# Performance work log

Hardware: AMD Instinct MI355X
Metric: run time of the kernel (lower is better)

The kernel has to match this reference:

```python
import jax, jax.numpy as jnp
import numpy as np

EPS_NORM = 1e-12   # torch F.normalize eps
EPS_TRIP = 1e-6    # torch pairwise_distance eps
MARGIN = 1.0

def _l2_normalize(x, axis=1):
    n = jnp.linalg.norm(x, axis=axis, keepdims=True)
    return x / jnp.maximum(n, EPS_NORM)

def setup_inputs() -> dict:
    key = jax.random.key(0)
    k1, k2 = jax.random.split(key)
    bs, m, d = 32768, 2048, 256
    query = jax.random.normal(k1, (bs, d), dtype=jnp.float32)
    memory = jax.random.normal(k2, (m, d), dtype=jnp.float32)
    return {"query": query, "memory": memory}

def reference(query, memory):
    m, d = memory.shape
    q = _l2_normalize(query, axis=1)                      # [bs, d]
    score = jnp.matmul(q, memory.T)                       # [bs, m]
    sfx_score_query = jax.nn.softmax(score, axis=0)       # softmax over batch
    sfx_score_memory = jax.nn.softmax(score, axis=1)      # softmax over slots

    # --- update (note: original passes sfx_score_query for BOTH score args) ---
    max_idx = jnp.argmax(sfx_score_query, axis=1)         # [bs] topk(k=1) over dim=1
    colmax = jnp.max(sfx_score_query, axis=0)             # [m]
    sel = jnp.take_along_axis(sfx_score_query, max_idx[:, None], axis=1)[:, 0]  # score[j, max_idx[j]]
    w = sel / colmax[max_idx]                              # [bs]
    # vectorized form of the per-slot gather/weighted-sum loop (segment-sum)
    query_update = jax.ops.segment_sum(w[:, None] * q, max_idx, num_segments=m)  # [m, d]
    updated_memory = jax.lax.stop_gradient(_l2_normalize(query_update + memory, axis=1))

    # --- read (uses ORIGINAL memory in the train path) ---
    concat_memory = jnp.matmul(jax.lax.stop_gradient(sfx_score_memory), memory)  # [bs, d]
    update_query = jnp.concatenate([q, concat_memory], axis=1)                   # [bs, 2d]

    # --- losses (computed from sfx_score_memory as intended) ---
    top2_vals, top2_idx = jax.lax.top_k(sfx_score_memory, 2)
    pos = jax.lax.stop_gradient(memory[top2_idx[:, 0]])   # [bs, d]
    neg = jax.lax.stop_gradient(memory[top2_idx[:, 1]])   # [bs, d]
    gathering_loss = jnp.mean((q - pos) ** 2)
    d_pos = jnp.linalg.norm(q - pos + EPS_TRIP, axis=1)
    d_neg = jnp.linalg.norm(q - neg + EPS_TRIP, axis=1)
    spreading_loss = jnp.mean(jnp.maximum(d_pos - d_neg + MARGIN, 0.0))

    return (update_query, updated_memory, sfx_score_query, sfx_score_memory,
            gathering_loss, spreading_loss)
```

## Files before the change

kernel.cpp:

```cpp
#include <hip/hip_runtime.h>
#include <hip/hip_bf16.h>
#include <cstddef>
#include <cstdint>

#define BS 32768
#define MSLOT 2048
#define D 256
#define NCHUNK 128

typedef _Float16 f16;
typedef _Float16 f16x8 __attribute__((ext_vector_type(8)));
typedef float f32x4 __attribute__((ext_vector_type(4)));

#define WAITV(n) asm volatile("s_waitcnt vmcnt(" #n ")" ::: "memory")

__device__ __forceinline__ void barrier_raw() {
    asm volatile("" ::: "memory");
    __builtin_amdgcn_s_barrier();
    asm volatile("" ::: "memory");
}

__device__ __forceinline__ void lds_cp16(void* dst, const void* src) {
    __builtin_amdgcn_global_load_lds(
        (const __attribute__((address_space(1))) void*)src,
        (__attribute__((address_space(3))) void*)dst, 16, 0, 0);
}

__device__ __forceinline__ void top2_merge(float& a0, int& ai0, float& a1, int& ai1,
                                           float b0, int bi0, float b1, int bi1)
{
    bool bt = (b0 > a0) || (b0 == a0 && bi0 < ai0);
    float n0, n1; int ni0, ni1;
    if (bt) {
        n0 = b0; ni0 = bi0;
        bool s2 = (b1 > a0) || (b1 == a0 && bi1 < ai0);
        n1 = s2 ? b1 : a0; ni1 = s2 ? bi1 : ai0;
    } else {
        n0 = a0; ni0 = ai0;
        bool s2 = (b0 > a1) || (b0 == a1 && bi0 < ai1);
        n1 = s2 ? b0 : a1; ni1 = s2 ? bi0 : ai1;
    }
    a0 = n0; ai0 = ni0; a1 = n1; ai1 = ni1;
}

__global__ __launch_bounds__(256) void k_prepq(const float* __restrict__ query,
                                               float* __restrict__ out0,
                                               f16* __restrict__ qcat)
{
    __shared__ float sbuf[4];
    const int i = blockIdx.x, t = threadIdx.x;
    float v = query[(size_t)i * D + t];
    float ss = v * v;
#pragma unroll
    for (int off = 32; off; off >>= 1) ss += __shfl_xor(ss, off, 64);
    if ((t & 63) == 0) sbuf[t >> 6] = ss;
    __syncthreads();
    float tot = (sbuf[0] + sbuf[1]) + (sbuf[2] + sbuf[3]);
    float n = fmaxf(sqrtf(tot), 1e-12f);
    float qv = v / n;
    out0[(size_t)i * (2 * D) + t] = qv;
    float qs = qv * 256.0f;
    f16 h = (f16)qs;
    f16 lo = (f16)(qs - (float)h);
    qcat[(size_t)i * 512 + t] = h;
    qcat[(size_t)i * 512 + 256 + t] = lo;
}

__global__ __launch_bounds__(256) void k_prepm(const float* __restrict__ memory,
                                               f16* __restrict__ mcat,
                                               f16* __restrict__ memT,
                                               float* __restrict__ qupd)
{
    const int j = blockIdx.x, t = threadIdx.x;
    float m = memory[(size_t)j * D + t];
    f16 h = (f16)m;
    f16 lo = (f16)(m - (float)h);
    mcat[(size_t)j * 512 + t] = h;
    mcat[(size_t)j * 512 + 256 + t] = lo;
    memT[(size_t)t * MSLOT + j] = h;
    qupd[(size_t)j * D + t] = 0.0f;
}

__global__ __launch_bounds__(512, 2) void k_score(const f16* __restrict__ qcat,
                                                  const f16* __restrict__ mcat,
                                                  float* __restrict__ out2,
                                                  float* __restrict__ colpart)
{
    __shared__ __align__(16) f16 As[2][256 * 64];
    __shared__ __align__(16) f16 Bs[2][256 * 64];
    __shared__ float sepM[8][4][16], sepS[8][4][16];

    const int tid = threadIdx.x;
    const int l = tid & 63, w = tid >> 6;
    const int wr = w >> 2, wc = w & 3;
    const int lk = (l >> 4) & 3, lm = l & 15;
    const int sr = tid >> 3, sch = tid & 7;

    const int hflat = blockIdx.y * 8 + blockIdx.x;
    const int xcd = hflat & 7, kk8 = hflat >> 3;
    const int by = xcd * 16 + (kk8 >> 3);
    const int bx = kk8 & 7;
    const int i0 = by * 256, j0 = bx * 256;

#define STAGE(buf, t) do {                                                          \
    int k0_ = (t) * 64;                                                             \
    int ao_ = ((t) < 8 ? 0 : 256) + (k0_ & 255);                                    \
    int bo_ = ((((t) >= 4) && ((t) < 8)) ? 256 : 0) + (k0_ & 255);                  \
    _Pragma("unroll")                                                               \
    for (int c = 0; c < 4; ++c) {                                                   \
        int r_ = c * 64 + sr;                                                       \
        int g_ = sch ^ ((r_ >> 1) & 7);                                             \
        lds_cp16(&As[buf][(c * 512 + tid) * 8],                                     \
                 qcat + (size_t)(i0 + r_) * 512 + ao_ + g_ * 8);                    \
        lds_cp16(&Bs[buf][(c * 512 + tid) * 8],                                     \
                 mcat + (size_t)(j0 + r_) * 512 + bo_ + g_ * 8);                    \
    }                                                                               \
} while (0)

    f32x4 acc[8][4] = {};

    STAGE(0, 0);
    STAGE(1, 1);

    for (int t = 0; t < 12; ++t) {
        const int cur = t & 1;
        if (t < 11) { WAITV(8); } else { WAITV(0); }
        barrier_raw();
        const f16* Ab = As[cur];
        const f16* Bb = Bs[cur];
        __builtin_amdgcn_s_setprio(1);
#pragma unroll
        for (int kk = 0; kk < 2; ++kk) {
            f16x8 bf[4];
#pragma unroll
            for (int ni = 0; ni < 4; ++ni) {
                int r = wc * 64 + ni * 16 + lm;
                int slot = (kk * 4 + lk) ^ (lm >> 1);
                bf[ni] = *(const f16x8*)(Bb + r * 64 + slot * 8);
            }
#pragma unroll
            for (int mi = 0; mi < 8; ++mi) {
                int r = wr * 128 + mi * 16 + lm;
                int slot = (kk * 4 + lk) ^ (lm >> 1);
                f16x8 af = *(const f16x8*)(Ab + r * 64 + slot * 8);
#pragma unroll
                for (int ni = 0; ni < 4; ++ni)
                    acc[mi][ni] = __builtin_amdgcn_mfma_f32_16x16x32_f16(af, bf[ni], acc[mi][ni], 0, 0, 0);
            }
        }
        __builtin_amdgcn_s_setprio(0);
        barrier_raw();
        if (t < 10) STAGE(cur, t + 2);
    }
#undef STAGE

    const float sc = 1.0f / 256.0f;
#pragma unroll
    for (int mi = 0; mi < 8; ++mi)
#pragma unroll
        for (int ni = 0; ni < 4; ++ni)
            acc[mi][ni] *= sc;

#pragma unroll
    for (int mi = 0; mi < 8; ++mi) {
        int row = i0 + wr * 128 + mi * 16 + lk * 4;
#pragma unroll
        for (int ni = 0; ni < 4; ++ni) {
            int col = j0 + wc * 64 + ni * 16 + lm;
#pragma unroll
            for (int r = 0; r < 4; ++r)
                out2[(size_t)(row + r) * MSLOT + col] = acc[mi][ni][r];
        }
    }

    float cm[4], cs[4];
#pragma unroll
    for (int ni = 0; ni < 4; ++ni) {
        float mx = -INFINITY;
#pragma unroll
        for (int mi = 0; mi < 8; ++mi)
#pragma unroll
            for (int r = 0; r < 4; ++r) mx = fmaxf(mx, acc[mi][ni][r]);
        float sm = 0.0f;
#pragma unroll
        for (int mi = 0; mi < 8; ++mi)
#pragma unroll
            for (int r = 0; r < 4; ++r) sm += __expf(acc[mi][ni][r] - mx);
#pragma unroll
        for (int off = 16; off <= 32; off <<= 1) {
            float om = __shfl_xor(mx, off, 64);
            float os = __shfl_xor(sm, off, 64);
            float nm = fmaxf(mx, om);
            sm = sm * __expf(mx - nm) + os * __expf(om - nm);
            mx = nm;
        }
        cm[ni] = mx; cs[ni] = sm;
    }
    if (l < 16) {
#pragma unroll
        for (int ni = 0; ni < 4; ++ni) { sepM[w][ni][l] = cm[ni]; sepS[w][ni][l] = cs[ni]; }
    }
    __syncthreads();
    if (w < 4 && l < 16) {
#pragma unroll
        for (int ni = 0; ni < 4; ++ni) {
            float m1 = sepM[w][ni][l], s1 = sepS[w][ni][l];
            float m2 = sepM[w + 4][ni][l], s2 = sepS[w + 4][ni][l];
            float nm = fmaxf(m1, m2);
            float ns = s1 * __expf(m1 - nm) + s2 * __expf(m2 - nm);
            int col = j0 + w * 64 + ni * 16 + l;
            size_t o = ((size_t)by * MSLOT + col) * 2;
            colpart[o + 0] = nm;
            colpart[o + 1] = ns;
        }
    }
}

__global__ __launch_bounds__(256) void k_colmerge(const float* __restrict__ colpart,
                                                  float* __restrict__ colM,
                                                  float* __restrict__ colSinv,
                                                  float* __restrict__ colC)
{
    const int col = blockIdx.x * 256 + threadIdx.x;
    float m = -INFINITY, s = 0.0f;
    for (int c = 0; c < NCHUNK; ++c) {
        size_t o = ((size_t)c * MSLOT + col) * 2;
        float pm = colpart[o + 0], ps = colpart[o + 1];
        float nm = fmaxf(m, pm);
        s = s * __expf(m - nm) + ps * __expf(pm - nm);
        m = nm;
    }
    colM[col] = m;
    colSinv[col] = 1.0f / s;
    colC[col] = m + __logf(s);
}

__global__ __launch_bounds__(256) void k_rowtrans(float* __restrict__ sq,
                                                  float* __restrict__ sm,
                                                  f16* __restrict__ pf16,
                                                  const float* __restrict__ colM,
                                                  const float* __restrict__ colSinv,
                                                  const float* __restrict__ colC,
                                                  const float* __restrict__ out0,
                                                  const float* __restrict__ memory,
                                                  int* __restrict__ jstarA, float* __restrict__ wA,
                                                  float* __restrict__ gpart, float* __restrict__ spart)
{
    __shared__ float swm[4], sws[4];
    __shared__ float st0v[4], st1v[4]; __shared__ int st0i[4], st1i[4];
    __shared__ float sav[4], sar[4];  __shared__ int sai[4];
    __shared__ float sg[4], sdp[4], sdn[4];

    const int i = blockIdx.x, t = threadIdx.x;
    const int l = t & 63, w = t >> 6;
    const int jb = t * 8;
    float* row = sq + (size_t)i * MSLOT;

    float v[8];
    {
        float4 va = *(const float4*)(row + jb);
        float4 vb = *(const float4*)(row + jb + 4);
        v[0] = va.x; v[1] = va.y; v[2] = va.z; v[3] = va.w;
        v[4] = vb.x; v[5] = vb.y; v[6] = vb.z; v[7] = vb.w;
    }
    float cCv[8], cMv[8], cSv[8];
    {
        float4 a = *(const float4*)(colC + jb);
        float4 b = *(const float4*)(colC + jb + 4);
        cCv[0] = a.x; cCv[1] = a.y; cCv[2] = a.z; cCv[3] = a.w;
        cCv[4] = b.x; cCv[5] = b.y; cCv[6] = b.z; cCv[7] = b.w;
        a = *(const float4*)(colM + jb); b = *(const float4*)(colM + jb + 4);
        cMv[0] = a.x; cMv[1] = a.y; cMv[2] = a.z; cMv[3] = a.w;
        cMv[4] = b.x; cMv[5] = b.y; cMv[6] = b.z; cMv[7] = b.w;
        a = *(const float4*)(colSinv + jb); b = *(const float4*)(colSinv + jb + 4);
        cSv[0] = a.x; cSv[1] = a.y; cSv[2] = a.z; cSv[3] = a.w;
        cSv[4] = b.x; cSv[5] = b.y; cSv[6] = b.z; cSv[7] = b.w;
    }

    float lmx = v[0];
#pragma unroll
    for (int k = 1; k < 8; ++k) lmx = fmaxf(lmx, v[k]);
#pragma unroll
    for (int off = 32; off; off >>= 1) lmx = fmaxf(lmx, __shfl_xor(lmx, off, 64));
    if (l == 0) swm[w] = lmx;
    __syncthreads();
    const float rm = fmaxf(fmaxf(swm[0], swm[1]), fmaxf(swm[2], swm[3]));

    float ls = 0.0f;
#pragma unroll
    for (int k = 0; k < 8; ++k) ls += __expf(v[k] - rm);

    float v0 = -INFINITY, v1 = -INFINITY; int i0 = 0x7fffffff, i1 = 0x7fffffff;
#pragma unroll
    for (int k = 0; k < 8; ++k) {
        int idx = jb + k; float cv = v[k];
        if (cv > v0)      { v1 = v0; i1 = i0; v0 = cv; i0 = idx; }
        else if (cv > v1) { v1 = cv; i1 = idx; }
    }

    float av = -INFINITY, araw = 0.0f; int ai = 0x7fffffff;
#pragma unroll
    for (int k = 0; k < 8; ++k) {
        int idx = jb + k;
        float x = v[k] - cCv[k];
        if (x > av) { av = x; ai = idx; araw = v[k]; }
    }

#pragma unroll
    for (int off = 32; off; off >>= 1) ls += __shfl_xor(ls, off, 64);
#pragma unroll
    for (int off = 1; off < 64; off <<= 1) {
        float b0 = __shfl_xor(v0, off, 64), b1 = __shfl_xor(v1, off, 64);
        int  bi0 = __shfl_xor(i0, off, 64), bi1 = __shfl_xor(i1, off, 64);
        top2_merge(v0, i0, v1, i1, b0, bi0, b1, bi1);
    }
#pragma unroll
    for (int off = 1; off < 64; off <<= 1) {
        float ov = __shfl_xor(av, off, 64), oraw = __shfl_xor(araw, off, 64);
        int   oi = __shfl_xor(ai, off, 64);
        if (ov > av || (ov == av && oi < ai)) { av = ov; ai = oi; araw = oraw; }
    }
    if (l == 0) {
        sws[w] = ls;
        st0v[w] = v0; st0i[w] = i0; st1v[w] = v1; st1i[w] = i1;
        sav[w] = av; sai[w] = ai; sar[w] = araw;
    }
    __syncthreads();

    const float rs = (sws[0] + sws[1]) + (sws[2] + sws[3]);
    const float rsinv = 1.0f / rs;

    float T0 = -INFINITY, T1 = -INFINITY; int I0 = 0x7fffffff, I1 = 0x7fffffff;
#pragma unroll
    for (int ww = 0; ww < 4; ++ww)
        top2_merge(T0, I0, T1, I1, st0v[ww], st0i[ww], st1v[ww], st1i[ww]);

    float AV = -INFINITY, AR = 0.0f; int AI = 0x7fffffff;
#pragma unroll
    for (int ww = 0; ww < 4; ++ww) {
        if (sav[ww] > AV || (sav[ww] == AV && sai[ww] < AI)) { AV = sav[ww]; AI = sai[ww]; AR = sar[ww]; }
    }

    float qv = out0[(size_t)i * (2 * D) + t];
    float pv = memory[(size_t)I0 * D + t];
    float nv = memory[(size_t)I1 * D + t];
    float dq = qv - pv;
    float g  = dq * dq;
    float dp = dq + 1e-6f;          dp *= dp;
    float dn = (qv - nv) + 1e-6f;   dn *= dn;
#pragma unroll
    for (int off = 32; off; off >>= 1) {
        g  += __shfl_xor(g, off, 64);
        dp += __shfl_xor(dp, off, 64);
        dn += __shfl_xor(dn, off, 64);
    }
    if (l == 0) { sg[w] = g; sdp[w] = dp; sdn[w] = dn; }
    __syncthreads();
    if (t == 0) {
        float gs  = (sg[0] + sg[1]) + (sg[2] + sg[3]);
        float dps = (sdp[0] + sdp[1]) + (sdp[2] + sdp[3]);
        float dns = (sdn[0] + sdn[1]) + (sdn[2] + sdn[3]);
        gpart[i] = gs;
        spart[i] = fmaxf(sqrtf(dps) - sqrtf(dns) + 1.0f, 0.0f);
        jstarA[i] = AI;
        wA[i] = __expf(AR - colM[AI]);
    }

    float oq[8], om[8];
#pragma unroll
    for (int k = 0; k < 8; ++k) {
        oq[k] = __expf(v[k] - cMv[k]) * cSv[k];
        om[k] = __expf(v[k] - rm) * rsinv;
    }
    float4 q0 = {oq[0], oq[1], oq[2], oq[3]}, q1 = {oq[4], oq[5], oq[6], oq[7]};
    float4 m0 = {om[0], om[1], om[2], om[3]}, m1 = {om[4], om[5], om[6], om[7]};
    *(float4*)(row + jb) = q0;
    *(float4*)(row + jb + 4) = q1;
    *(float4*)(sm + (size_t)i * MSLOT + jb) = m0;
    *(float4*)(sm + (size_t)i * MSLOT + jb + 4) = m1;
    f16x8 h;
#pragma unroll
    for (int k = 0; k < 8; ++k) h[k] = (f16)om[k];
    *(f16x8*)(pf16 + (size_t)i * MSLOT + jb) = h;
}

__global__ __launch_bounds__(256) void k_scatter(const f16* __restrict__ qcat,
                                                 const int* __restrict__ jstarA,
                                                 const float* __restrict__ wA,
                                                 float* __restrict__ qupd)
{
    const int i = blockIdx.x, t = threadIdx.x;
    const int j = jstarA[i];
    const float wv = wA[i] * (1.0f / 256.0f);
    float qv = (float)qcat[(size_t)i * 512 + t] + (float)qcat[(size_t)i * 512 + 256 + t];
    unsafeAtomicAdd(&qupd[(size_t)j * D + t], wv * qv);
}

__global__ __launch_bounds__(256) void k_updmem(const float* __restrict__ qupd,
                                                const float* __restrict__ memory,
                                                float* __restrict__ out1)
{
    __shared__ float sbuf[4];
    const int j = blockIdx.x, t = threadIdx.x;
    float v = qupd[(size_t)j * D + t] + memory[(size_t)j * D + t];
    float ss = v * v;
#pragma unroll
    for (int off = 32; off; off >>= 1) ss += __shfl_xor(ss, off, 64);
    if ((t & 63) == 0) sbuf[t >> 6] = ss;
    __syncthreads();
    float tot = (sbuf[0] + sbuf[1]) + (sbuf[2] + sbuf[3]);
    float n = fmaxf(sqrtf(tot), 1e-12f);
    out1[(size_t)j * D + t] = v / n;
}

__global__ __launch_bounds__(512, 2) void k_concat(const f16* __restrict__ P,
                                                   const f16* __restrict__ memT,
                                                   float* __restrict__ out0)
{
    __shared__ __align__(16) f16 As[2][128 * 64];
    __shared__ __align__(16) f16 Bs[2][256 * 64];
    const int tid = threadIdx.x;
    const int l = tid & 63, w = tid >> 6;
    const int wr = w >> 2, wc = w & 3;
    const int lk = (l >> 4) & 3, lm = l & 15;
    const int sr = tid >> 3, sch = tid & 7;
    const int i0 = blockIdx.x * 128;

#define STAGE_CC(buf, t) do {                                                       \
    int k0_ = (t) * 64;                                                             \
    _Pragma("unroll")                                                               \
    for (int c = 0; c < 2; ++c) {                                                   \
        int r_ = c * 64 + sr;                                                       \
        int g_ = sch ^ ((r_ >> 1) & 7);                                             \
        lds_cp16(&As[buf][(c * 512 + tid) * 8],                                     \
                 P + (size_t)(i0 + r_) * MSLOT + k0_ + g_ * 8);                     \
    }                                                                               \
    _Pragma("unroll")                                                               \
    for (int c = 0; c < 4; ++c) {                                                   \
        int r_ = c * 64 + sr;                                                       \
        int g_ = sch ^ ((r_ >> 1) & 7);                                             \
        lds_cp16(&Bs[buf][(c * 512 + tid) * 8],                                     \
                 memT + (size_t)r_ * MSLOT + k0_ + g_ * 8);                         \
    }                                                                               \
} while (0)

    f32x4 acc[4][4] = {};

    STAGE_CC(0, 0);
    STAGE_CC(1, 1);

    for (int t = 0; t < 32; ++t) {
        const int cur = t & 1;
        if (t < 31) { WAITV(6); } else { WAITV(0); }
        barrier_raw();
        const f16* Ab = As[cur];
        const f16* Bb = Bs[cur];
        __builtin_amdgcn_s_setprio(1);
#pragma unroll
        for (int kk = 0; kk < 2; ++kk) {
            f16x8 bf[4];
#pragma unroll
            for (int ni = 0; ni < 4; ++ni) {
                int r = wc * 64 + ni * 16 + lm;
                int slot = (kk * 4 + lk) ^ (lm >> 1);
                bf[ni] = *(const f16x8*)(Bb + r * 64 + slot * 8);
            }
#pragma unroll
            for (int mi = 0; mi < 4; ++mi) {
                int r = wr * 64 + mi * 16 + lm;
                int slot = (kk * 4 + lk) ^ (lm >> 1);
                f16x8 af = *(const f16x8*)(Ab + r * 64 + slot * 8);
#pragma unroll
                for (int ni = 0; ni < 4; ++ni)
                    acc[mi][ni] = __builtin_amdgcn_mfma_f32_16x16x32_f16(af, bf[ni], acc[mi][ni], 0, 0, 0);
            }
        }
        __builtin_amdgcn_s_setprio(0);
        barrier_raw();
        if (t < 30) STAGE_CC(cur, t + 2);
    }
#undef STAGE_CC

#pragma unroll
    for (int mi = 0; mi < 4; ++mi) {
        int row = i0 + wr * 64 + mi * 16 + lk * 4;
#pragma unroll
        for (int ni = 0; ni < 4; ++ni) {
            int col = wc * 64 + ni * 16 + lm;
#pragma unroll
            for (int r = 0; r < 4; ++r)
                out0[(size_t)(row + r) * (2 * D) + D + col] = acc[mi][ni][r];
        }
    }
}

__global__ __launch_bounds__(256) void k_losses(const float* __restrict__ gpart,
                                                const float* __restrict__ spart,
                                                float* __restrict__ out45)
{
    __shared__ float sf[256];
    const int t = threadIdx.x;
    float g = 0.f, s = 0.f;
    for (int i = t; i < BS; i += 256) { g += gpart[i]; s += spart[i]; }
    sf[t] = g; __syncthreads();
    for (int off = 128; off; off >>= 1) { if (t < off) sf[t] += sf[t + off]; __syncthreads(); }
    float gt = sf[0]; __syncthreads();
    sf[t] = s; __syncthreads();
    for (int off = 128; off; off >>= 1) { if (t < off) sf[t] += sf[t + off]; __syncthreads(); }
    float st = sf[0];
    if (t == 0) {
        out45[0] = gt / (float)((size_t)BS * D);
        out45[1] = st / (float)BS;
    }
}

extern "C" void kernel_launch(void* const* d_in, const int* in_sizes, int n_in,
                              void* d_out, int out_size, void* d_ws, size_t ws_size,
                              hipStream_t stream)
{
    const float* query  = (const float*)d_in[0];
    const float* memory = (const float*)d_in[1];

    float* out  = (float*)d_out;
    float* out0 = out;
    float* out1 = out0 + (size_t)BS * 2 * D;
    float* out2 = out1 + (size_t)MSLOT * D;
    float* out3 = out2 + (size_t)BS * MSLOT;
    float* out45 = out3 + (size_t)BS * MSLOT;

    f16* qcat = (f16*)d_ws;
    f16* mcat = qcat + (size_t)BS * 512;
    f16* memT = mcat + (size_t)MSLOT * 512;
    f16* pf16 = memT + (size_t)D * MSLOT;
    float* colpart = (float*)(pf16 + (size_t)BS * MSLOT);
    float* colM    = colpart + (size_t)NCHUNK * MSLOT * 2;
    float* colSinv = colM + MSLOT;
    float* colC    = colSinv + MSLOT;
    float* wA      = colC + MSLOT;
    int*   jstarA  = (int*)(wA + BS);
    float* gpart   = (float*)(jstarA + BS);
    float* spart   = gpart + BS;
    float* qupd    = spart + BS;

    k_prepq<<<BS, 256, 0, stream>>>(query, out0, qcat);
    k_prepm<<<MSLOT, 256, 0, stream>>>(memory, mcat, memT, qupd);

    k_score<<<dim3(MSLOT / 256, BS / 256), 512, 0, stream>>>(qcat, mcat, out2, colpart);

    k_colmerge<<<MSLOT / 256, 256, 0, stream>>>(colpart, colM, colSinv, colC);

    k_rowtrans<<<BS, 256, 0, stream>>>(out2, out3, pf16, colM, colSinv, colC, out0, memory,
                                       jstarA, wA, gpart, spart);

    k_scatter<<<BS, 256, 0, stream>>>(qcat, jstarA, wA, qupd);
    k_updmem<<<MSLOT, 256, 0, stream>>>(qupd, memory, out1);

    k_concat<<<BS / 128, 512, 0, stream>>>(pf16, memT, out0);

    k_losses<<<1, 256, 0, stream>>>(gpart, spart, out45);
}
```

Measured before the change: 578.2 us.

## Fuse row softmax transform with probability-times-memory matmul, drop fp16 P buffer

Merges the per-row softmax/top-2/loss kernel with the concat GEMM. Each block handles 64 rows: a first pass computes an online row max/sum, top-2 and the argmax statistics, and a second pass rereads the score rows, writes both softmax outputs, and puts fp16 probabilities straight into LDS for MFMA against memT. This removes the 128MB fp16 P write and reread and one launch. In exchange the score rows are read twice, the B tile is single-buffered with a barrier every k-step, and the M tile is smaller (64 rows), so memT is reloaded more often.

```diff
diff --git a/kernel.cpp b/kernel.cpp
--- a/kernel.cpp
+++ b/kernel.cpp
@@ -13,6 +13,7 @@
 typedef float f32x4 __attribute__((ext_vector_type(4)));
 
 #define WAITV(n) asm volatile("s_waitcnt vmcnt(" #n ")" ::: "memory")
+#define WAITLGKM asm volatile("s_waitcnt lgkmcnt(0)" ::: "memory")
 
 __device__ __forceinline__ void barrier_raw() {
     asm volatile("" ::: "memory");
@@ -235,153 +236,208 @@
     colC[col] = m + __logf(s);
 }
 
-__global__ __launch_bounds__(256) void k_rowtrans(float* __restrict__ sq,
-                                                  float* __restrict__ sm,
-                                                  f16* __restrict__ pf16,
-                                                  const float* __restrict__ colM,
-                                                  const float* __restrict__ colSinv,
-                                                  const float* __restrict__ colC,
-                                                  const float* __restrict__ out0,
-                                                  const float* __restrict__ memory,
-                                                  int* __restrict__ jstarA, float* __restrict__ wA,
-                                                  float* __restrict__ gpart, float* __restrict__ spart)
-{
-    __shared__ float swm[4], sws[4];
-    __shared__ float st0v[4], st1v[4]; __shared__ int st0i[4], st1i[4];
-    __shared__ float sav[4], sar[4];  __shared__ int sai[4];
-    __shared__ float sg[4], sdp[4], sdn[4];
-
-    const int i = blockIdx.x, t = threadIdx.x;
-    const int l = t & 63, w = t >> 6;
-    const int jb = t * 8;
-    float* row = sq + (size_t)i * MSLOT;
-
-    float v[8];
-    {
-        float4 va = *(const float4*)(row + jb);
-        float4 vb = *(const float4*)(row + jb + 4);
-        v[0] = va.x; v[1] = va.y; v[2] = va.z; v[3] = va.w;
-        v[4] = vb.x; v[5] = vb.y; v[6] = vb.z; v[7] = vb.w;
-    }
-    float cCv[8], cMv[8], cSv[8];
-    {
-        float4 a = *(const float4*)(colC + jb);
-        float4 b = *(const float4*)(colC + jb + 4);
-        cCv[0] = a.x; cCv[1] = a.y; cCv[2] = a.z; cCv[3] = a.w;
-        cCv[4] = b.x; cCv[5] = b.y; cCv[6] = b.z; cCv[7] = b.w;
-        a = *(const float4*)(colM + jb); b = *(const float4*)(colM + jb + 4);
-        cMv[0] = a.x; cMv[1] = a.y; cMv[2] = a.z; cMv[3] = a.w;
-        cMv[4] = b.x; cMv[5] = b.y; cMv[6] = b.z; cMv[7] = b.w;
-        a = *(const float4*)(colSinv + jb); b = *(const float4*)(colSinv + jb + 4);
-        cSv[0] = a.x; cSv[1] = a.y; cSv[2] = a.z; cSv[3] = a.w;
-        cSv[4] = b.x; cSv[5] = b.y; cSv[6] = b.z; cSv[7] = b.w;
-    }
-
-    float lmx = v[0];
-#pragma unroll
-    for (int k = 1; k < 8; ++k) lmx = fmaxf(lmx, v[k]);
-#pragma unroll
-    for (int off = 32; off; off >>= 1) lmx = fmaxf(lmx, __shfl_xor(lmx, off, 64));
-    if (l == 0) swm[w] = lmx;
-    __syncthreads();
-    const float rm = fmaxf(fmaxf(swm[0], swm[1]), fmaxf(swm[2], swm[3]));
-
-    float ls = 0.0f;
-#pragma unroll
-    for (int k = 0; k < 8; ++k) ls += __expf(v[k] - rm);
-
-    float v0 = -INFINITY, v1 = -INFINITY; int i0 = 0x7fffffff, i1 = 0x7fffffff;
-#pragma unroll
-    for (int k = 0; k < 8; ++k) {
-        int idx = jb + k; float cv = v[k];
-        if (cv > v0)      { v1 = v0; i1 = i0; v0 = cv; i0 = idx; }
-        else if (cv > v1) { v1 = cv; i1 = idx; }
-    }
-
+__global__ __launch_bounds__(512, 2) void k_transcat(float* out2,
+                                                     float* __restrict__ out3,
+                                                     float* __restrict__ out0,
+                                                     const f16* __restrict__ memT,
+                                                     const float* __restrict__ colM,
+                                                     const float* __restrict__ colSinv,
+                                                     const float* __restrict__ colC,
+                                                     const float* __restrict__ memory,
+                                                     int* __restrict__ jstarA, float* __restrict__ wA,
+                                                     float* __restrict__ gpart, float* __restrict__ spart)
+{
+    __shared__ __align__(16) f16 Atile[64 * 128];
+    __shared__ __align__(16) f16 Btile[256 * 128];
+
+    const int tid = threadIdx.x;
+    const int l = tid & 63, w = tid >> 6;
+    const int wr = w >> 2, wc = w & 3;
+    const int lk = (l >> 4) & 3, lm = l & 15;
+    const int rl = tid >> 3, q8 = tid & 7;
+    const int grow = blockIdx.x * 64 + rl;
+    float* srow = out2 + (size_t)grow * MSLOT;
+
+    float pm = -INFINITY, ps = 0.0f;
+    float t0v = -INFINITY, t1v = -INFINITY; int t0i = 0x7fffffff, t1i = 0x7fffffff;
     float av = -INFINITY, araw = 0.0f; int ai = 0x7fffffff;
-#pragma unroll
-    for (int k = 0; k < 8; ++k) {
-        int idx = jb + k;
-        float x = v[k] - cCv[k];
-        if (x > av) { av = x; ai = idx; araw = v[k]; }
-    }
-
-#pragma unroll
-    for (int off = 32; off; off >>= 1) ls += __shfl_xor(ls, off, 64);
-#pragma unroll
-    for (int off = 1; off < 64; off <<= 1) {
-        float b0 = __shfl_xor(v0, off, 64), b1 = __shfl_xor(v1, off, 64);
-        int  bi0 = __shfl_xor(i0, off, 64), bi1 = __shfl_xor(i1, off, 64);
-        top2_merge(v0, i0, v1, i1, b0, bi0, b1, bi1);
-    }
-#pragma unroll
-    for (int off = 1; off < 64; off <<= 1) {
+
+    for (int kc = 0; kc < 16; ++kc) {
+        const int c0 = kc * 128 + q8 * 16;
+        float xv[16], cc[16];
+#pragma unroll
+        for (int u = 0; u < 4; ++u) {
+            float4 a = *(const float4*)(srow + c0 + u * 4);
+            xv[u * 4 + 0] = a.x; xv[u * 4 + 1] = a.y; xv[u * 4 + 2] = a.z; xv[u * 4 + 3] = a.w;
+            float4 b = *(const float4*)(colC + c0 + u * 4);
+            cc[u * 4 + 0] = b.x; cc[u * 4 + 1] = b.y; cc[u * 4 + 2] = b.z; cc[u * 4 + 3] = b.w;
+        }
+        float lmax = xv[0];
+#pragma unroll
+        for (int u = 1; u < 16; ++u) lmax = fmaxf(lmax, xv[u]);
+        float nm = fmaxf(pm, lmax);
+        ps *= __expf(pm - nm);
+        pm = nm;
+#pragma unroll
+        for (int u = 0; u < 16; ++u) ps += __expf(xv[u] - pm);
+#pragma unroll
+        for (int u = 0; u < 16; ++u) {
+            int idx = c0 + u; float cv = xv[u];
+            if (cv > t0v)      { t1v = t0v; t1i = t0i; t0v = cv; t0i = idx; }
+            else if (cv > t1v) { t1v = cv; t1i = idx; }
+            float x = cv - cc[u];
+            if (x > av) { av = x; ai = idx; araw = cv; }
+        }
+    }
+#pragma unroll
+    for (int off = 1; off < 8; off <<= 1) {
+        float opm = __shfl_xor(pm, off, 64), ops = __shfl_xor(ps, off, 64);
+        float nm = fmaxf(pm, opm);
+        ps = ps * __expf(pm - nm) + ops * __expf(opm - nm);
+        pm = nm;
+        float b0 = __shfl_xor(t0v, off, 64), b1 = __shfl_xor(t1v, off, 64);
+        int  bi0 = __shfl_xor(t0i, off, 64), bi1 = __shfl_xor(t1i, off, 64);
+        top2_merge(t0v, t0i, t1v, t1i, b0, bi0, b1, bi1);
         float ov = __shfl_xor(av, off, 64), oraw = __shfl_xor(araw, off, 64);
         int   oi = __shfl_xor(ai, off, 64);
         if (ov > av || (ov == av && oi < ai)) { av = ov; ai = oi; araw = oraw; }
     }
-    if (l == 0) {
-        sws[w] = ls;
-        st0v[w] = v0; st0i[w] = i0; st1v[w] = v1; st1i[w] = i1;
-        sav[w] = av; sai[w] = ai; sar[w] = araw;
-    }
-    __syncthreads();
-
-    const float rs = (sws[0] + sws[1]) + (sws[2] + sws[3]);
-    const float rsinv = 1.0f / rs;
-
-    float T0 = -INFINITY, T1 = -INFINITY; int I0 = 0x7fffffff, I1 = 0x7fffffff;
-#pragma unroll
-    for (int ww = 0; ww < 4; ++ww)
-        top2_merge(T0, I0, T1, I1, st0v[ww], st0i[ww], st1v[ww], st1i[ww]);
-
-    float AV = -INFINITY, AR = 0.0f; int AI = 0x7fffffff;
-#pragma unroll
-    for (int ww = 0; ww < 4; ++ww) {
-        if (sav[ww] > AV || (sav[ww] == AV && sai[ww] < AI)) { AV = sav[ww]; AI = sai[ww]; AR = sar[ww]; }
-    }
-
-    float qv = out0[(size_t)i * (2 * D) + t];
-    float pv = memory[(size_t)I0 * D + t];
-    float nv = memory[(size_t)I1 * D + t];
-    float dq = qv - pv;
-    float g  = dq * dq;
-    float dp = dq + 1e-6f;          dp *= dp;
-    float dn = (qv - nv) + 1e-6f;   dn *= dn;
-#pragma unroll
-    for (int off = 32; off; off >>= 1) {
-        g  += __shfl_xor(g, off, 64);
-        dp += __shfl_xor(dp, off, 64);
-        dn += __shfl_xor(dn, off, 64);
-    }
-    if (l == 0) { sg[w] = g; sdp[w] = dp; sdn[w] = dn; }
-    __syncthreads();
-    if (t == 0) {
-        float gs  = (sg[0] + sg[1]) + (sg[2] + sg[3]);
-        float dps = (sdp[0] + sdp[1]) + (sdp[2] + sdp[3]);
-        float dns = (sdn[0] + sdn[1]) + (sdn[2] + sdn[3]);
-        gpart[i] = gs;
-        spart[i] = fmaxf(sqrtf(dps) - sqrtf(dns) + 1.0f, 0.0f);
-        jstarA[i] = AI;
-        wA[i] = __expf(AR - colM[AI]);
-    }
-
-    float oq[8], om[8];
-#pragma unroll
-    for (int k = 0; k < 8; ++k) {
-        oq[k] = __expf(v[k] - cMv[k]) * cSv[k];
-        om[k] = __expf(v[k] - rm) * rsinv;
-    }
-    float4 q0 = {oq[0], oq[1], oq[2], oq[3]}, q1 = {oq[4], oq[5], oq[6], oq[7]};
-    float4 m0 = {om[0], om[1], om[2], om[3]}, m1 = {om[4], om[5], om[6], om[7]};
-    *(float4*)(row + jb) = q0;
-    *(float4*)(row + jb + 4) = q1;
-    *(float4*)(sm + (size_t)i * MSLOT + jb) = m0;
-    *(float4*)(sm + (size_t)i * MSLOT + jb + 4) = m1;
-    f16x8 h;
-#pragma unroll
-    for (int k = 0; k < 8; ++k) h[k] = (f16)om[k];
-    *(f16x8*)(pf16 + (size_t)i * MSLOT + jb) = h;
+    const float rm = pm;
+    const float rsinv = 1.0f / ps;
+
+    {
+        float g = 0.0f, dp = 0.0f, dn = 0.0f;
+        const float* qrow = out0 + (size_t)grow * (2 * D) + q8 * 32;
+        const float* prow = memory + (size_t)t0i * D + q8 * 32;
+        const float* nrow = memory + (size_t)t1i * D + q8 * 32;
+#pragma unroll
+        for (int u = 0; u < 8; ++u) {
+            float4 qv = *(const float4*)(qrow + u * 4);
+            float4 pv = *(const float4*)(prow + u * 4);
+            float4 nv = *(const float4*)(nrow + u * 4);
+#pragma unroll
+            for (int e = 0; e < 4; ++e) {
+                float qe = ((const float*)&qv)[e];
+                float pe = ((const float*)&pv)[e];
+                float ne = ((const float*)&nv)[e];
+                float dq = qe - pe;
+                g += dq * dq;
+                float a = dq + 1e-6f;        dp += a * a;
+                float b = (qe - ne) + 1e-6f; dn += b * b;
+            }
+        }
+#pragma unroll
+        for (int off = 1; off < 8; off <<= 1) {
+            g  += __shfl_xor(g, off, 64);
+            dp += __shfl_xor(dp, off, 64);
+            dn += __shfl_xor(dn, off, 64);
+        }
+        if (q8 == 0) {
+            gpart[grow] = g;
+            spart[grow] = fmaxf(sqrtf(dp) - sqrtf(dn) + 1.0f, 0.0f);
+            jstarA[grow] = ai;
+            wA[grow] = __expf(araw - colM[ai]);
+        }
+    }
+
+    f32x4 acc[2][4] = {};
+    const int i0row = blockIdx.x * 64;
+
+    for (int kc = 0; kc < 16; ++kc) {
+        barrier_raw();
+        const int c0 = kc * 128 + q8 * 16;
+
+        float4 s0 = *(const float4*)(srow + c0 + 0);
+        float4 s1 = *(const float4*)(srow + c0 + 4);
+        float4 s2 = *(const float4*)(srow + c0 + 8);
+        float4 s3 = *(const float4*)(srow + c0 + 12);
+
+#pragma unroll
+        for (int c = 0; c < 8; ++c) {
+            int f = c * 512 + tid;
+            int n = f >> 4, s = f & 15;
+            int g = s ^ (n & 15);
+            lds_cp16(&Btile[f * 8], memT + (size_t)n * MSLOT + kc * 128 + g * 8);
+        }
+
+        float v[16];
+        v[0] = s0.x; v[1] = s0.y; v[2] = s0.z; v[3] = s0.w;
+        v[4] = s1.x; v[5] = s1.y; v[6] = s1.z; v[7] = s1.w;
+        v[8] = s2.x; v[9] = s2.y; v[10] = s2.z; v[11] = s2.w;
+        v[12] = s3.x; v[13] = s3.y; v[14] = s3.z; v[15] = s3.w;
+
+        float cM[16], cS[16];
+#pragma unroll
+        for (int u = 0; u < 4; ++u) {
+            float4 a = *(const float4*)(colM + c0 + u * 4);
+            cM[u * 4 + 0] = a.x; cM[u * 4 + 1] = a.y; cM[u * 4 + 2] = a.z; cM[u * 4 + 3] = a.w;
+            float4 b = *(const float4*)(colSinv + c0 + u * 4);
+            cS[u * 4 + 0] = b.x; cS[u * 4 + 1] = b.y; cS[u * 4 + 2] = b.z; cS[u * 4 + 3] = b.w;
+        }
+
+        float oq[16], om[16];
+#pragma unroll
+        for (int u = 0; u < 16; ++u) {
+            oq[u] = __expf(v[u] - cM[u]) * cS[u];
+            om[u] = __expf(v[u] - rm) * rsinv;
+        }
+        float4 w0 = {oq[0], oq[1], oq[2], oq[3]},  w1 = {oq[4], oq[5], oq[6], oq[7]};
+        float4 w2 = {oq[8], oq[9], oq[10], oq[11]}, w3 = {oq[12], oq[13], oq[14], oq[15]};
+        *(float4*)(srow + c0 + 0) = w0;  *(float4*)(srow + c0 + 4) = w1;
+        *(float4*)(srow + c0 + 8) = w2;  *(float4*)(srow + c0 + 12) = w3;
+        float4 m0 = {om[0], om[1], om[2], om[3]},  m1 = {om[4], om[5], om[6], om[7]};
+        float4 m2 = {om[8], om[9], om[10], om[11]}, m3 = {om[12], om[13], om[14], om[15]};
+        float* mrow = out3 + (size_t)grow * MSLOT + c0;
+        *(float4*)(mrow + 0) = m0;  *(float4*)(mrow + 4) = m1;
+        *(float4*)(mrow + 8) = m2;  *(float4*)(mrow + 12) = m3;
+
+        f16x8 h0, h1;
+#pragma unroll
+        for (int u = 0; u < 8; ++u) { h0[u] = (f16)om[u]; h1[u] = (f16)om[u + 8]; }
+        int sw0 = (q8 * 2 + 0) ^ (rl & 15);
+        int sw1 = (q8 * 2 + 1) ^ (rl & 15);
+        *(f16x8*)(Atile + rl * 128 + sw0 * 8) = h0;
+        *(f16x8*)(Atile + rl * 128 + sw1 * 8) = h1;
+
+        WAITLGKM;
+        WAITV(8);
+        barrier_raw();
+        __builtin_amdgcn_sched_barrier(0);
+
+        __builtin_amdgcn_s_setprio(1);
+#pragma unroll
+        for (int kk = 0; kk < 4; ++kk) {
+            f16x8 bf[4];
+#pragma unroll
+            for (int ni = 0; ni < 4; ++ni) {
+                int n = wc * 64 + ni * 16 + lm;
+                int slot = (kk * 4 + lk) ^ (n & 15);
+                bf[ni] = *(const f16x8*)(Btile + n * 128 + slot * 8);
+            }
+#pragma unroll
+            for (int mi = 0; mi < 2; ++mi) {
+                int r = wr * 32 + mi * 16 + lm;
+                int slot = (kk * 4 + lk) ^ (r & 15);
+                f16x8 af = *(const f16x8*)(Atile + r * 128 + slot * 8);
+#pragma unroll
+                for (int ni = 0; ni < 4; ++ni)
+                    acc[mi][ni] = __builtin_amdgcn_mfma_f32_16x16x32_f16(af, bf[ni], acc[mi][ni], 0, 0, 0);
+            }
+        }
+        __builtin_amdgcn_s_setprio(0);
+    }
+
+#pragma unroll
+    for (int mi = 0; mi < 2; ++mi) {
+        int row = i0row + wr * 32 + mi * 16 + lk * 4;
+#pragma unroll
+        for (int ni = 0; ni < 4; ++ni) {
+            int col = wc * 64 + ni * 16 + lm;
+#pragma unroll
+            for (int r = 0; r < 4; ++r)
+                out0[(size_t)(row + r) * (2 * D) + D + col] = acc[mi][ni][r];
+        }
+    }
 }
 
 __global__ __launch_bounds__(256) void k_scatter(const f16* __restrict__ qcat,
@@ -411,87 +467,6 @@
     float tot = (sbuf[0] + sbuf[1]) + (sbuf[2] + sbuf[3]);
     float n = fmaxf(sqrtf(tot), 1e-12f);
     out1[(size_t)j * D + t] = v / n;
-}
-
-__global__ __launch_bounds__(512, 2) void k_concat(const f16* __restrict__ P,
-                                                   const f16* __restrict__ memT,
-                                                   float* __restrict__ out0)
-{
-    __shared__ __align__(16) f16 As[2][128 * 64];
-    __shared__ __align__(16) f16 Bs[2][256 * 64];
-    const int tid = threadIdx.x;
-    const int l = tid & 63, w = tid >> 6;
-    const int wr = w >> 2, wc = w & 3;
-    const int lk = (l >> 4) & 3, lm = l & 15;
-    const int sr = tid >> 3, sch = tid & 7;
-    const int i0 = blockIdx.x * 128;
-
-#define STAGE_CC(buf, t) do {                                                       \
-    int k0_ = (t) * 64;                                                             \
-    _Pragma("unroll")                                                               \
-    for (int c = 0; c < 2; ++c) {                                                   \
-        int r_ = c * 64 + sr;                                                       \
-        int g_ = sch ^ ((r_ >> 1) & 7);                                             \
-        lds_cp16(&As[buf][(c * 512 + tid) * 8],                                     \
-                 P + (size_t)(i0 + r_) * MSLOT + k0_ + g_ * 8);                     \
-    }                                                                               \
-    _Pragma("unroll")                                                               \
-    for (int c = 0; c < 4; ++c) {                                                   \
-        int r_ = c * 64 + sr;                                                       \
-        int g_ = sch ^ ((r_ >> 1) & 7);                                             \
-        lds_cp16(&Bs[buf][(c * 512 + tid) * 8],                                     \
-                 memT + (size_t)r_ * MSLOT + k0_ + g_ * 8);                         \
-    }                                                                               \
-} while (0)
-
-    f32x4 acc[4][4] = {};
-
-    STAGE_CC(0, 0);
-    STAGE_CC(1, 1);
-
-    for (int t = 0; t < 32; ++t) {
-        const int cur = t & 1;
-        if (t < 31) { WAITV(6); } else { WAITV(0); }
-        barrier_raw();
-        const f16* Ab = As[cur];
-        const f16* Bb = Bs[cur];
-        __builtin_amdgcn_s_setprio(1);
-#pragma unroll
-        for (int kk = 0; kk < 2; ++kk) {
-            f16x8 bf[4];
-#pragma unroll
-            for (int ni = 0; ni < 4; ++ni) {
-                int r = wc * 64 + ni * 16 + lm;
-                int slot = (kk * 4 + lk) ^ (lm >> 1);
-                bf[ni] = *(const f16x8*)(Bb + r * 64 + slot * 8);
-            }
-#pragma unroll
-            for (int mi = 0; mi < 4; ++mi) {
-                int r = wr * 64 + mi * 16 + lm;
-                int slot = (kk * 4 + lk) ^ (lm >> 1);
-                f16x8 af = *(const f16x8*)(Ab + r * 64 + slot * 8);
-#pragma unroll
-                for (int ni = 0; ni < 4; ++ni)
-                    acc[mi][ni] = __builtin_amdgcn_mfma_f32_16x16x32_f16(af, bf[ni], acc[mi][ni], 0, 0, 0);
-            }
-        }
-        __builtin_amdgcn_s_setprio(0);
-        barrier_raw();
-        if (t < 30) STAGE_CC(cur, t + 2);
-    }
-#undef STAGE_CC
-
-#pragma unroll
-    for (int mi = 0; mi < 4; ++mi) {
-        int row = i0 + wr * 64 + mi * 16 + lk * 4;
-#pragma unroll
-        for (int ni = 0; ni < 4; ++ni) {
-            int col = wc * 64 + ni * 16 + lm;
-#pragma unroll
-            for (int r = 0; r < 4; ++r)
-                out0[(size_t)(row + r) * (2 * D) + D + col] = acc[mi][ni][r];
-        }
-    }
 }
 
 __global__ __launch_bounds__(256) void k_losses(const float* __restrict__ gpart,
@@ -531,8 +506,7 @@
     f16* qcat = (f16*)d_ws;
     f16* mcat = qcat + (size_t)BS * 512;
     f16* memT = mcat + (size_t)MSLOT * 512;
-    f16* pf16 = memT + (size_t)D * MSLOT;
-    float* colpart = (float*)(pf16 + (size_t)BS * MSLOT);
+    float* colpart = (float*)(memT + (size_t)D * MSLOT);
     float* colM    = colpart + (size_t)NCHUNK * MSLOT * 2;
     float* colSinv = colM + MSLOT;
     float* colC    = colSinv + MSLOT;
@@ -549,13 +523,12 @@
 
     k_colmerge<<<MSLOT / 256, 256, 0, stream>>>(colpart, colM, colSinv, colC);
 
-    k_rowtrans<<<BS, 256, 0, stream>>>(out2, out3, pf16, colM, colSinv, colC, out0, memory,
-                                       jstarA, wA, gpart, spart);
+    k_transcat<<<BS / 64, 512, 0, stream>>>(out2, out3, out0, memT,
+                                            colM, colSinv, colC, memory,
+                                            jstarA, wA, gpart, spart);
 
     k_scatter<<<BS, 256, 0, stream>>>(qcat, jstarA, wA, qupd);
     k_updmem<<<MSLOT, 256, 0, stream>>>(qupd, memory, out1);
 
-    k_concat<<<BS / 128, 512, 0, stream>>>(pf16, memT, out0);
-
     k_losses<<<1, 256, 0, stream>>>(gpart, spart, out45);
 }
```

Measured after the change: 591.4 us. 2.3% more time.

## Triple-buffer GEMM pipelines and shrink score tile to 256x128

Applied to the files above, without the earlier changes.

Both MFMA GEMM kernels (score and concat) switch from double to triple buffering in LDS. Each iteration now drops the trailing barrier, issues the next-next stage's global-to-LDS loads in two halves interleaved with the two k-substeps, and loads A and B fragments ahead of the MFMA bursts. The score kernel's block tile shrinks from 256x256 to 256x128 with a 4x2 wave layout, using a 1D grid of 2048 blocks with XCD-aware remapping, and the column-softmax partial merge now combines four waves instead of two. This aims to hide load latency and improve occupancy and CU balance, at the cost of more LDS use in the concat kernel and more redundant A loads in the score kernel.

```diff
diff --git a/kernel.cpp b/kernel.cpp
--- a/kernel.cpp
+++ b/kernel.cpp
@@ -86,84 +86,108 @@
                                                   float* __restrict__ out2,
                                                   float* __restrict__ colpart)
 {
-    __shared__ __align__(16) f16 As[2][256 * 64];
-    __shared__ __align__(16) f16 Bs[2][256 * 64];
+    __shared__ __align__(16) f16 As[3][256 * 64];
+    __shared__ __align__(16) f16 Bs[3][128 * 64];
     __shared__ float sepM[8][4][16], sepS[8][4][16];
 
     const int tid = threadIdx.x;
     const int l = tid & 63, w = tid >> 6;
-    const int wr = w >> 2, wc = w & 3;
+    const int wr = w >> 1, wc = w & 1;
     const int lk = (l >> 4) & 3, lm = l & 15;
-    const int sr = tid >> 3, sch = tid & 7;
-
-    const int hflat = blockIdx.y * 8 + blockIdx.x;
-    const int xcd = hflat & 7, kk8 = hflat >> 3;
-    const int by = xcd * 16 + (kk8 >> 3);
-    const int bx = kk8 & 7;
-    const int i0 = by * 256, j0 = bx * 256;
-
-#define STAGE(buf, t) do {                                                          \
-    int k0_ = (t) * 64;                                                             \
-    int ao_ = ((t) < 8 ? 0 : 256) + (k0_ & 255);                                    \
-    int bo_ = ((((t) >= 4) && ((t) < 8)) ? 256 : 0) + (k0_ & 255);                  \
-    _Pragma("unroll")                                                               \
-    for (int c = 0; c < 4; ++c) {                                                   \
-        int r_ = c * 64 + sr;                                                       \
-        int g_ = sch ^ ((r_ >> 1) & 7);                                             \
-        lds_cp16(&As[buf][(c * 512 + tid) * 8],                                     \
-                 qcat + (size_t)(i0 + r_) * 512 + ao_ + g_ * 8);                    \
-        lds_cp16(&Bs[buf][(c * 512 + tid) * 8],                                     \
-                 mcat + (size_t)(j0 + r_) * 512 + bo_ + g_ * 8);                    \
-    }                                                                               \
+    const int sch = tid & 7;
+
+    const int g = blockIdx.x;
+    const int xcd = g & 7, r8 = g >> 3;
+    const int by = xcd * 16 + (r8 & 15);
+    const int bx = r8 >> 4;
+    const int i0 = by * 256, j0 = bx * 128;
+
+#define SC_A(buf, T, c) do {                                                        \
+    int k0_ = (T) * 64;                                                             \
+    int ao_ = ((T) < 8 ? 0 : 256) + (k0_ & 255);                                    \
+    int f_ = (c) * 512 + tid;                                                       \
+    int r_ = f_ >> 3;                                                               \
+    int g_ = sch ^ ((r_ >> 1) & 7);                                                 \
+    lds_cp16(&As[buf][f_ * 8], qcat + (size_t)(i0 + r_) * 512 + ao_ + g_ * 8);      \
 } while (0)
-
-    f32x4 acc[8][4] = {};
-
-    STAGE(0, 0);
-    STAGE(1, 1);
-
-    for (int t = 0; t < 12; ++t) {
-        const int cur = t & 1;
-        if (t < 11) { WAITV(8); } else { WAITV(0); }
+#define SC_B(buf, T, c) do {                                                        \
+    int k0_ = (T) * 64;                                                             \
+    int bo_ = ((((T) >= 4) && ((T) < 8)) ? 256 : 0) + (k0_ & 255);                  \
+    int f_ = (c) * 512 + tid;                                                       \
+    int r_ = f_ >> 3;                                                               \
+    int g_ = sch ^ ((r_ >> 1) & 7);                                                 \
+    lds_cp16(&Bs[buf][f_ * 8], mcat + (size_t)(j0 + r_) * 512 + bo_ + g_ * 8);      \
+} while (0)
+
+    f32x4 acc[4][4] = {};
+
+    SC_A(0, 0, 0); SC_A(0, 0, 1); SC_A(0, 0, 2); SC_A(0, 0, 3); SC_B(0, 0, 0); SC_B(0, 0, 1);
+    SC_A(1, 1, 0); SC_A(1, 1, 1); SC_A(1, 1, 2); SC_A(1, 1, 3); SC_B(1, 1, 0); SC_B(1, 1, 1);
+
+    for (int T = 0; T < 12; ++T) {
+        const int buf = T % 3;
+        const int nbuf = (T + 2) % 3;
+        if (T < 11) { WAITV(6); } else { WAITV(0); }
         barrier_raw();
-        const f16* Ab = As[cur];
-        const f16* Bb = Bs[cur];
-        __builtin_amdgcn_s_setprio(1);
-#pragma unroll
-        for (int kk = 0; kk < 2; ++kk) {
-            f16x8 bf[4];
+        const f16* Ab = As[buf];
+        const f16* Bb = Bs[buf];
+
+        if (T < 10) { SC_A(nbuf, T + 2, 0); SC_A(nbuf, T + 2, 1); SC_B(nbuf, T + 2, 0); }
+        {
+            f16x8 bf[4], af[4];
 #pragma unroll
             for (int ni = 0; ni < 4; ++ni) {
-                int r = wc * 64 + ni * 16 + lm;
-                int slot = (kk * 4 + lk) ^ (lm >> 1);
-                bf[ni] = *(const f16x8*)(Bb + r * 64 + slot * 8);
-            }
-#pragma unroll
-            for (int mi = 0; mi < 8; ++mi) {
-                int r = wr * 128 + mi * 16 + lm;
-                int slot = (kk * 4 + lk) ^ (lm >> 1);
-                f16x8 af = *(const f16x8*)(Ab + r * 64 + slot * 8);
+                int rr = wc * 64 + ni * 16 + lm;
+                bf[ni] = *(const f16x8*)(Bb + rr * 64 + (lk ^ (lm >> 1)) * 8);
+            }
+#pragma unroll
+            for (int mi = 0; mi < 4; ++mi) {
+                int rr = wr * 64 + mi * 16 + lm;
+                af[mi] = *(const f16x8*)(Ab + rr * 64 + (lk ^ (lm >> 1)) * 8);
+            }
+            __builtin_amdgcn_s_setprio(1);
+#pragma unroll
+            for (int mi = 0; mi < 4; ++mi)
 #pragma unroll
                 for (int ni = 0; ni < 4; ++ni)
-                    acc[mi][ni] = __builtin_amdgcn_mfma_f32_16x16x32_f16(af, bf[ni], acc[mi][ni], 0, 0, 0);
-            }
-        }
-        __builtin_amdgcn_s_setprio(0);
-        barrier_raw();
-        if (t < 10) STAGE(cur, t + 2);
-    }
-#undef STAGE
+                    acc[mi][ni] = __builtin_amdgcn_mfma_f32_16x16x32_f16(af[mi], bf[ni], acc[mi][ni], 0, 0, 0);
+            __builtin_amdgcn_s_setprio(0);
+        }
+        if (T < 10) { SC_A(nbuf, T + 2, 2); SC_A(nbuf, T + 2, 3); SC_B(nbuf, T + 2, 1); }
+        {
+            f16x8 bf[4], af[4];
+#pragma unroll
+            for (int ni = 0; ni < 4; ++ni) {
+                int rr = wc * 64 + ni * 16 + lm;
+                bf[ni] = *(const f16x8*)(Bb + rr * 64 + ((4 + lk) ^ (lm >> 1)) * 8);
+            }
+#pragma unroll
+            for (int mi = 0; mi < 4; ++mi) {
+                int rr = wr * 64 + mi * 16 + lm;
+                af[mi] = *(const f16x8*)(Ab + rr * 64 + ((4 + lk) ^ (lm >> 1)) * 8);
+            }
+            __builtin_amdgcn_s_setprio(1);
+#pragma unroll
+            for (int mi = 0; mi < 4; ++mi)
+#pragma unroll
+                for (int ni = 0; ni < 4; ++ni)
+                    acc[mi][ni] = __builtin_amdgcn_mfma_f32_16x16x32_f16(af[mi], bf[ni], acc[mi][ni], 0, 0, 0);
+            __builtin_amdgcn_s_setprio(0);
+        }
+    }
+#undef SC_A
+#undef SC_B
 
     const float sc = 1.0f / 256.0f;
 #pragma unroll
-    for (int mi = 0; mi < 8; ++mi)
+    for (int mi = 0; mi < 4; ++mi)
 #pragma unroll
         for (int ni = 0; ni < 4; ++ni)
             acc[mi][ni] *= sc;
 
 #pragma unroll
-    for (int mi = 0; mi < 8; ++mi) {
-        int row = i0 + wr * 128 + mi * 16 + lk * 4;
+    for (int mi = 0; mi < 4; ++mi) {
+        int row = i0 + wr * 64 + mi * 16 + lk * 4;
 #pragma unroll
         for (int ni = 0; ni < 4; ++ni) {
             int col = j0 + wc * 64 + ni * 16 + lm;
@@ -178,12 +202,12 @@
     for (int ni = 0; ni < 4; ++ni) {
         float mx = -INFINITY;
 #pragma unroll
-        for (int mi = 0; mi < 8; ++mi)
+        for (int mi = 0; mi < 4; ++mi)
 #pragma unroll
             for (int r = 0; r < 4; ++r) mx = fmaxf(mx, acc[mi][ni][r]);
         float sm = 0.0f;
 #pragma unroll
-        for (int mi = 0; mi < 8; ++mi)
+        for (int mi = 0; mi < 4; ++mi)
 #pragma unroll
             for (int r = 0; r < 4; ++r) sm += __expf(acc[mi][ni][r] - mx);
 #pragma unroll
@@ -201,17 +225,21 @@
         for (int ni = 0; ni < 4; ++ni) { sepM[w][ni][l] = cm[ni]; sepS[w][ni][l] = cs[ni]; }
     }
     __syncthreads();
-    if (w < 4 && l < 16) {
+    if (w < 2 && l < 16) {
 #pragma unroll
         for (int ni = 0; ni < 4; ++ni) {
             float m1 = sepM[w][ni][l], s1 = sepS[w][ni][l];
-            float m2 = sepM[w + 4][ni][l], s2 = sepS[w + 4][ni][l];
-            float nm = fmaxf(m1, m2);
-            float ns = s1 * __expf(m1 - nm) + s2 * __expf(m2 - nm);
+#pragma unroll
+            for (int u = 1; u < 4; ++u) {
+                float m2 = sepM[w + 2 * u][ni][l], s2 = sepS[w + 2 * u][ni][l];
+                float nm = fmaxf(m1, m2);
+                s1 = s1 * __expf(m1 - nm) + s2 * __expf(m2 - nm);
+                m1 = nm;
+            }
             int col = j0 + w * 64 + ni * 16 + l;
             size_t o = ((size_t)by * MSLOT + col) * 2;
-            colpart[o + 0] = nm;
-            colpart[o + 1] = ns;
+            colpart[o + 0] = m1;
+            colpart[o + 1] = s1;
         }
     }
 }
@@ -417,69 +445,86 @@
                                                    const f16* __restrict__ memT,
                                                    float* __restrict__ out0)
 {
-    __shared__ __align__(16) f16 As[2][128 * 64];
-    __shared__ __align__(16) f16 Bs[2][256 * 64];
+    __shared__ __align__(16) f16 As[3][128 * 64];
+    __shared__ __align__(16) f16 Bs[3][256 * 64];
     const int tid = threadIdx.x;
     const int l = tid & 63, w = tid >> 6;
     const int wr = w >> 2, wc = w & 3;
     const int lk = (l >> 4) & 3, lm = l & 15;
-    const int sr = tid >> 3, sch = tid & 7;
+    const int sch = tid & 7;
     const int i0 = blockIdx.x * 128;
 
-#define STAGE_CC(buf, t) do {                                                       \
-    int k0_ = (t) * 64;                                                             \
-    _Pragma("unroll")                                                               \
-    for (int c = 0; c < 2; ++c) {                                                   \
-        int r_ = c * 64 + sr;                                                       \
-        int g_ = sch ^ ((r_ >> 1) & 7);                                             \
-        lds_cp16(&As[buf][(c * 512 + tid) * 8],                                     \
-                 P + (size_t)(i0 + r_) * MSLOT + k0_ + g_ * 8);                     \
-    }                                                                               \
-    _Pragma("unroll")                                                               \
-    for (int c = 0; c < 4; ++c) {                                                   \
-        int r_ = c * 64 + sr;                                                       \
-        int g_ = sch ^ ((r_ >> 1) & 7);                                             \
-        lds_cp16(&Bs[buf][(c * 512 + tid) * 8],                                     \
-                 memT + (size_t)r_ * MSLOT + k0_ + g_ * 8);                         \
-    }                                                                               \
+#define CC_A(buf, T, c) do {                                                        \
+    int f_ = (c) * 512 + tid;                                                       \
+    int r_ = f_ >> 3;                                                               \
+    int g_ = sch ^ ((r_ >> 1) & 7);                                                 \
+    lds_cp16(&As[buf][f_ * 8], P + (size_t)(i0 + r_) * MSLOT + (T) * 64 + g_ * 8);  \
 } while (0)
+#define CC_B(buf, T, c) do {                                                        \
+    int f_ = (c) * 512 + tid;                                                       \
+    int r_ = f_ >> 3;                                                               \
+    int g_ = sch ^ ((r_ >> 1) & 7);                                                 \
+    lds_cp16(&Bs[buf][f_ * 8], memT + (size_t)r_ * MSLOT + (T) * 64 + g_ * 8);      \
+} while (0)
 
     f32x4 acc[4][4] = {};
 
-    STAGE_CC(0, 0);
-    STAGE_CC(1, 1);
-
-    for (int t = 0; t < 32; ++t) {
-        const int cur = t & 1;
-        if (t < 31) { WAITV(6); } else { WAITV(0); }
+    CC_A(0, 0, 0); CC_A(0, 0, 1); CC_B(0, 0, 0); CC_B(0, 0, 1); CC_B(0, 0, 2); CC_B(0, 0, 3);
+    CC_A(1, 1, 0); CC_A(1, 1, 1); CC_B(1, 1, 0); CC_B(1, 1, 1); CC_B(1, 1, 2); CC_B(1, 1, 3);
+
+    for (int T = 0; T < 32; ++T) {
+        const int buf = T % 3;
+        const int nbuf = (T + 2) % 3;
+        if (T < 31) { WAITV(6); } else { WAITV(0); }
         barrier_raw();
-        const f16* Ab = As[cur];
-        const f16* Bb = Bs[cur];
-        __builtin_amdgcn_s_setprio(1);
-#pragma unroll
-        for (int kk = 0; kk < 2; ++kk) {
-            f16x8 bf[4];
+        const f16* Ab = As[buf];
+        const f16* Bb = Bs[buf];
+
+        if (T < 30) { CC_A(nbuf, T + 2, 0); CC_B(nbuf, T + 2, 0); CC_B(nbuf, T + 2, 1); }
+        {
+            f16x8 bf[4], af[4];
 #pragma unroll
             for (int ni = 0; ni < 4; ++ni) {
-                int r = wc * 64 + ni * 16 + lm;
-                int slot = (kk * 4 + lk) ^ (lm >> 1);
-                bf[ni] = *(const f16x8*)(Bb + r * 64 + slot * 8);
+                int rr = wc * 64 + ni * 16 + lm;
+                bf[ni] = *(const f16x8*)(Bb + rr * 64 + (lk ^ (lm >> 1)) * 8);
             }
 #pragma unroll
             for (int mi = 0; mi < 4; ++mi) {
-                int r = wr * 64 + mi * 16 + lm;
-                int slot = (kk * 4 + lk) ^ (lm >> 1);
-                f16x8 af = *(const f16x8*)(Ab + r * 64 + slot * 8);
+                int rr = wr * 64 + mi * 16 + lm;
+                af[mi] = *(const f16x8*)(Ab + rr * 64 + (lk ^ (lm >> 1)) * 8);
+            }
+            __builtin_amdgcn_s_setprio(1);
+#pragma unroll
+            for (int mi = 0; mi < 4; ++mi)
 #pragma unroll
                 for (int ni = 0; ni < 4; ++ni)
-                    acc[mi][ni] = __builtin_amdgcn_mfma_f32_16x16x32_f16(af, bf[ni], acc[mi][ni], 0, 0, 0);
-            }
-        }
-        __builtin_amdgcn_s_setprio(0);
-        barrier_raw();
-        if (t < 30) STAGE_CC(cur, t + 2);
-    }
-#undef STAGE_CC
+                    acc[mi][ni] = __builtin_amdgcn_mfma_f32_16x16x32_f16(af[mi], bf[ni], acc[mi][ni], 0, 0, 0);
+            __builtin_amdgcn_s_setprio(0);
+        }
+        if (T < 30) { CC_A(nbuf, T + 2, 1); CC_B(nbuf, T + 2, 2); CC_B(nbuf, T + 2, 3); }
+        {
+            f16x8 bf[4], af[4];
+#pragma unroll
+            for (int ni = 0; ni < 4; ++ni) {
+                int rr = wc * 64 + ni * 16 + lm;
+                bf[ni] = *(const f16x8*)(Bb + rr * 64 + ((4 + lk) ^ (lm >> 1)) * 8);
+            }
+#pragma unroll
+            for (int mi = 0; mi < 4; ++mi) {
+                int rr = wr * 64 + mi * 16 + lm;
+                af[mi] = *(const f16x8*)(Ab + rr * 64 + ((4 + lk) ^ (lm >> 1)) * 8);
+            }
+            __builtin_amdgcn_s_setprio(1);
+#pragma unroll
+            for (int mi = 0; mi < 4; ++mi)
+#pragma unroll
+                for (int ni = 0; ni < 4; ++ni)
+                    acc[mi][ni] = __builtin_amdgcn_mfma_f32_16x16x32_f16(af[mi], bf[ni], acc[mi][ni], 0, 0, 0);
+            __builtin_amdgcn_s_setprio(0);
+        }
+    }
+#undef CC_A
+#undef CC_B
 
 #pragma unroll
     for (int mi = 0; mi < 4; ++mi) {
@@ -545,7 +590,7 @@
     k_prepq<<<BS, 256, 0, stream>>>(query, out0, qcat);
     k_prepm<<<MSLOT, 256, 0, stream>>>(memory, mcat, memT, qupd);
 
-    k_score<<<dim3(MSLOT / 256, BS / 256), 512, 0, stream>>>(qcat, mcat, out2, colpart);
+    k_score<<<2048, 512, 0, stream>>>(qcat, mcat, out2, colpart);
 
     k_colmerge<<<MSLOT / 256, 256, 0, stream>>>(colpart, colM, colSinv, colC);
 
```

Result: slower. 636.5 us (+10.1%).
